# Kernel optimization log

Hardware: AMD Instinct MI355X
Metric: run time of the kernel (lower is better)

The kernel has to match this reference:

```python
import jax, jax.numpy as jnp
import numpy as np

EPS = 1e-08
STRIDE = (2, 2)
INV_SQRT2 = np.float32(1.0 / np.sqrt(2.0))
INV_SQRT_2PI = np.float32(1.0 / np.sqrt(2.0 * np.pi))


def _neigh(t, r, s, ho, wo):
    # t: [B, C, H, W]. Faithful to the torch conv: the CxC filter sums the
    # selected 2x2 pixel over ALL input channels and replicates it across
    # the C output channels.
    sh, sw = STRIDE
    sub = t[:, :, r::sh, s::sw][:, :, :ho, :wo]          # strided gather [B,C,ho,wo]
    summed = jnp.sum(sub, axis=1, keepdims=True)          # channel sum [B,1,ho,wo]
    return jnp.broadcast_to(summed, sub.shape)            # [B,C,ho,wo]


def _max_gaussians_1d(m1, v1, m2, v2):
    alpha = jnp.sqrt(v1 + v2 + EPS)
    beta = (m1 - m2) / alpha
    cdf_b = 0.5 * (1.0 + jax.lax.erf(beta * INV_SQRT2))
    cdf_nb = 0.5 * (1.0 + jax.lax.erf(-beta * INV_SQRT2))
    pdf_b = jnp.exp(-0.5 * beta * beta) * INV_SQRT_2PI
    mean = m1 * cdf_b + m2 * cdf_nb + alpha * pdf_b
    var = ((v1 + m1 * m1) * cdf_b + (v2 + m2 * m2) * cdf_nb
           + (m1 + m2) * alpha * pdf_b - mean * mean + EPS)
    return mean, var


def setup_inputs() -> dict:
    key = jax.random.key(0)
    # uniform [0,1) so the variance plane (x[:,1]) is nonnegative
    x = jax.random.uniform(key, (32, 2, 128, 64, 64), dtype=jnp.float32)
    return {"x": x}


def reference(x):
    means, variances = x[:, 0], x[:, 1]                   # [B,C,H,W] each
    B, C, H, W = means.shape
    sh, sw = STRIDE
    ho = (H - 2) // sh + 1
    wo = (W - 2) // sw + 1
    # neighbors in order: 1|2 / 3|4
    offsets = [(0, 0), (0, 1), (1, 0), (1, 1)]
    nm = [_neigh(means, r, s, ho, wo) for (r, s) in offsets]
    nv = [_neigh(variances, r, s, ho, wo) for (r, s) in offsets]
    hm1, hv1 = _max_gaussians_1d(nm[0], nv[0], nm[1], nv[1])
    hm2, hv2 = _max_gaussians_1d(nm[2], nv[2], nm[3], nv[3])
    mean, var = _max_gaussians_1d(hm1, hv1, hm2, hv2)
    return jnp.stack([mean, var], axis=1)                 # [B,2,C,ho,wo]
```

## Files before the change

### kernel.cpp

```cpp
#include <hip/hip_runtime.h>
#include <math.h>

#define EPSF 1e-8f
#define INV_SQRT2F 0.70710678118654752f
#define INV_SQRT_2PIF 0.39894228040143268f

__device__ inline void max_gauss(float m1, float v1, float m2, float v2,
                                 float& mo, float& vo) {
    float alpha = sqrtf(v1 + v2 + EPSF);
    float beta  = (m1 - m2) / alpha;
    float e     = erff(beta * INV_SQRT2F);
    float cdf_b  = 0.5f * (1.0f + e);
    float cdf_nb = 0.5f * (1.0f - e);
    float pdf_b  = expf(-0.5f * beta * beta) * INV_SQRT_2PIF;
    mo = m1 * cdf_b + m2 * cdf_nb + alpha * pdf_b;
    vo = (v1 + m1 * m1) * cdf_b + (v2 + m2 * m2) * cdf_nb
       + (m1 + m2) * alpha * pdf_b - mo * mo + EPSF;
}

__global__ __launch_bounds__(256) void dmp_kernel(const float* __restrict__ x,
                                                  float* __restrict__ out) {
    const int C = 128;
    const size_t CH = 4096;

    int blk = blockIdx.x;
    int b = blk >> 5;
    int i = blk & 31;
    int t = threadIdx.x;
    int j = t & 31;
    int g = t >> 5;

    float a[8] = {0.f, 0.f, 0.f, 0.f, 0.f, 0.f, 0.f, 0.f};

    const float* mbase = x + ((size_t)b * 2) * C * CH + (size_t)(g * 16) * CH
                           + (size_t)(2 * i) * 64 + (size_t)(2 * j);
    const float* vbase = mbase + (size_t)C * CH;

    #pragma unroll 4
    for (int c = 0; c < 16; ++c) {
        const float* mp = mbase + (size_t)c * CH;
        const float* vp = vbase + (size_t)c * CH;
        float2 m0 = *(const float2*)(mp);
        float2 m1 = *(const float2*)(mp + 64);
        float2 v0 = *(const float2*)(vp);
        float2 v1 = *(const float2*)(vp + 64);
        a[0] += m0.x; a[1] += m0.y; a[2] += m1.x; a[3] += m1.y;
        a[4] += v0.x; a[5] += v0.y; a[6] += v1.x; a[7] += v1.y;
    }

    __shared__ float red[8][32][9];
    #pragma unroll
    for (int q = 0; q < 8; ++q) red[g][j][q] = a[q];
    __syncthreads();

    __shared__ float mv[2][32];
    if (t < 32) {
        float s[8];
        #pragma unroll
        for (int q = 0; q < 8; ++q) {
            float acc = 0.f;
            #pragma unroll
            for (int gg = 0; gg < 8; ++gg) acc += red[gg][t][q];
            s[q] = acc;
        }
        float hm1, hv1, hm2, hv2, m, v;
        max_gauss(s[0], s[4], s[1], s[5], hm1, hv1);
        max_gauss(s[2], s[6], s[3], s[7], hm2, hv2);
        max_gauss(hm1, hv1, hm2, hv2, m, v);
        mv[0][t] = m;
        mv[1][t] = v;
    }
    __syncthreads();

    #pragma unroll
    for (int it = 0; it < 8; ++it) {
        int idx = it * 256 + t;
        int u   = idx >> 10;
        int rem = idx & 1023;
        int c   = rem >> 3;
        int jq  = rem & 7;
        float4 val;
        val.x = mv[u][jq * 4 + 0];
        val.y = mv[u][jq * 4 + 1];
        val.z = mv[u][jq * 4 + 2];
        val.w = mv[u][jq * 4 + 3];
        size_t off = (((size_t)b * 2 + u) * C + c) * 1024 + (size_t)i * 32
                   + (size_t)(jq * 4);
        *(float4*)(out + off) = val;
    }
}

extern "C" void kernel_launch(void* const* d_in, const int* in_sizes, int n_in,
                              void* d_out, int out_size, void* d_ws, size_t ws_size,
                              hipStream_t stream) {
    const float* x = (const float*)d_in[0];
    float* out = (float*)d_out;
    dim3 grid(1024), block(256);
    hipLaunchKernelGGL(dmp_kernel, grid, block, 0, stream, x, out);
}
```

Before: 30.42 us.

## Use float4 loads with 512-thread blocks and restructure channel reduction

```diff
diff --git a/kernel.cpp b/kernel.cpp
--- a/kernel.cpp
+++ b/kernel.cpp
@@ -18,63 +18,70 @@
        + (m1 + m2) * alpha * pdf_b - mo * mo + EPSF;
 }
 
-__global__ __launch_bounds__(256) void dmp_kernel(const float* __restrict__ x,
+__global__ __launch_bounds__(512) void dmp_kernel(const float* __restrict__ x,
                                                   float* __restrict__ out) {
-    const int C = 128;
-    const size_t CH = 4096;
+    const size_t PL = 4096;
 
     int blk = blockIdx.x;
     int b = blk >> 5;
     int i = blk & 31;
     int t = threadIdx.x;
-    int j = t & 31;
+    int q = t & 31;
     int g = t >> 5;
+    int qp = q & 15;
+    int r  = q >> 4;
 
-    float a[8] = {0.f, 0.f, 0.f, 0.f, 0.f, 0.f, 0.f, 0.f};
+    const float* base = x + ((size_t)b * 256 + (size_t)g) * PL
+                          + (size_t)(2 * i + r) * 64 + (size_t)(4 * qp);
 
-    const float* mbase = x + ((size_t)b * 2) * C * CH + (size_t)(g * 16) * CH
-                           + (size_t)(2 * i) * 64 + (size_t)(2 * j);
-    const float* vbase = mbase + (size_t)C * CH;
+    float am[4] = {0.f, 0.f, 0.f, 0.f};
+    float av[4] = {0.f, 0.f, 0.f, 0.f};
 
-    #pragma unroll 4
-    for (int c = 0; c < 16; ++c) {
-        const float* mp = mbase + (size_t)c * CH;
-        const float* vp = vbase + (size_t)c * CH;
-        float2 m0 = *(const float2*)(mp);
-        float2 m1 = *(const float2*)(mp + 64);
-        float2 v0 = *(const float2*)(vp);
-        float2 v1 = *(const float2*)(vp + 64);
-        a[0] += m0.x; a[1] += m0.y; a[2] += m1.x; a[3] += m1.y;
-        a[4] += v0.x; a[5] += v0.y; a[6] += v1.x; a[7] += v1.y;
+    #pragma unroll
+    for (int it = 0; it < 16; ++it) {
+        float4 d = *(const float4*)(base + (size_t)it * 16 * PL);
+        if (it < 8) { am[0] += d.x; am[1] += d.y; am[2] += d.z; am[3] += d.w; }
+        else        { av[0] += d.x; av[1] += d.y; av[2] += d.z; av[3] += d.w; }
     }
 
-    __shared__ float red[8][32][9];
+    __shared__ float red[16][32][9];
     #pragma unroll
-    for (int q = 0; q < 8; ++q) red[g][j][q] = a[q];
+    for (int k = 0; k < 4; ++k) {
+        red[g][q][k]     = am[k];
+        red[g][q][4 + k] = av[k];
+    }
     __syncthreads();
 
     __shared__ float mv[2][32];
     if (t < 32) {
-        float s[8];
+        int j  = t;
+        int qh = j >> 1;
+        int o  = (j & 1) * 2;
+        float sm[2][2] = {{0.f, 0.f}, {0.f, 0.f}};
+        float sv[2][2] = {{0.f, 0.f}, {0.f, 0.f}};
         #pragma unroll
-        for (int q = 0; q < 8; ++q) {
-            float acc = 0.f;
+        for (int gg = 0; gg < 16; ++gg) {
             #pragma unroll
-            for (int gg = 0; gg < 8; ++gg) acc += red[gg][t][q];
-            s[q] = acc;
+            for (int rr = 0; rr < 2; ++rr) {
+                int qq = rr * 16 + qh;
+                sm[rr][0] += red[gg][qq][o];
+                sm[rr][1] += red[gg][qq][o + 1];
+                sv[rr][0] += red[gg][qq][4 + o];
+                sv[rr][1] += red[gg][qq][4 + o + 1];
+            }
         }
         float hm1, hv1, hm2, hv2, m, v;
-        max_gauss(s[0], s[4], s[1], s[5], hm1, hv1);
-        max_gauss(s[2], s[6], s[3], s[7], hm2, hv2);
+        max_gauss(sm[0][0], sv[0][0], sm[0][1], sv[0][1], hm1, hv1);
+        max_gauss(sm[1][0], sv[1][0], sm[1][1], sv[1][1], hm2, hv2);
         max_gauss(hm1, hv1, hm2, hv2, m, v);
-        mv[0][t] = m;
-        mv[1][t] = v;
+        mv[0][j] = m;
+        mv[1][j] = v;
     }
     __syncthreads();
 
     #pragma unroll
-    for (int it = 0; it < 8; ++it) {
-        int idx = it * 256 + t;
+    for (int w = 0; w < 4; ++w) {
+        int idx = w * 512 + t;
         int u   = idx >> 10;
         int rem = idx & 1023;
         int c   = rem >> 3;
@@ -84,8 +91,8 @@
         val.y = mv[u][jq * 4 + 1];
         val.z = mv[u][jq * 4 + 2];
         val.w = mv[u][jq * 4 + 3];
-        size_t off = (((size_t)b * 2 + u) * C + c) * 1024 + (size_t)i * 32
-                   + (size_t)(jq * 4);
+        size_t off = (((size_t)b * 2 + u) * 128 + (size_t)c) * 1024
+                   + (size_t)i * 32 + (size_t)(jq * 4);
         *(float4*)(out + off) = val;
     }
 }
@@ -95,6 +102,6 @@
                               hipStream_t stream) {
     const float* x = (const float*)d_in[0];
     float* out = (float*)d_out;
-    dim3 grid(1024), block(256);
+    dim3 grid(1024), block(512);
     hipLaunchKernelGGL(dmp_kernel, grid, block, 0, stream, x, out);
 }
```

Measured after the change: 30.63 us. Within noise of the previous version (+0.7%).
